# Performance work log

Hardware: AMD Instinct MI355X
Metric: run time of the kernel (lower is better)

Reference implementation:

```python
import jax, jax.numpy as jnp
import numpy as np

VOCAB, EMBED, HIDDEN = 32000, 256, 512
B, T = 8, 512


def setup_inputs() -> dict:
    key = jax.random.key(0)
    ks = jax.random.split(key, 7)
    x = jax.random.randint(ks[0], (B, T), 0, VOCAB)
    emb = jax.random.normal(ks[1], (VOCAB, EMBED), dtype=jnp.float32)
    W_xh = jax.random.normal(ks[2], (EMBED, HIDDEN), dtype=jnp.float32) * 0.01
    W_hh = jax.random.normal(ks[3], (HIDDEN, HIDDEN), dtype=jnp.float32) * 0.01
    b_h = jnp.zeros((HIDDEN,), dtype=jnp.float32)
    # nn.Linear(hidden*2, vocab): weight [vocab, 2*hidden], bias [vocab]
    lim = 1.0 / np.sqrt(2 * HIDDEN)
    fc_w = jax.random.uniform(ks[4], (VOCAB, 2 * HIDDEN), minval=-lim, maxval=lim, dtype=jnp.float32)
    fc_b = jax.random.uniform(ks[5], (VOCAB,), minval=-lim, maxval=lim, dtype=jnp.float32)
    return {"x": x, "emb": emb, "W_xh": W_xh, "W_hh": W_hh, "b_h": b_h, "fc_w": fc_w, "fc_b": fc_b}


def reference(x, emb, W_xh, W_hh, b_h, fc_w, fc_b):
    e = emb[x]  # [B,T,E]
    h0 = jnp.zeros((x.shape[0], W_hh.shape[0]), dtype=e.dtype)

    def step(h, xt):  # xt: [B,E]
        h = jnp.tanh(xt @ W_xh + h @ W_hh + b_h)
        return h, h

    _, H = jax.lax.scan(step, h0, jnp.swapaxes(e, 0, 1))  # H: [T,B,Hd]
    H = jnp.swapaxes(H, 0, 1)  # [B,T,Hd]
    # full (non-causal) dot-product self-attention over hidden states
    scores = jnp.einsum('bth,bsh->bts', H, H)  # [B,T,T]
    attn = jax.nn.softmax(scores, axis=-1)
    ctx = jnp.einsum('bts,bsh->bth', attn, H)  # [B,T,Hd]
    combined = jnp.concatenate([H, ctx], axis=-1)  # [B,T,2Hd]
    return combined @ fc_w.T + fc_b  # [B,T,V]
```

## Files before the change

kernel.cpp:

```cpp
#include <hip/hip_runtime.h>

typedef unsigned int u32;
typedef unsigned short u16;
typedef short bf16x8 __attribute__((ext_vector_type(8)));
typedef float f32x4 __attribute__((ext_vector_type(4)));

#define DEV __device__ __forceinline__

DEV u16 f2bf(float f) {
  u32 u = __builtin_bit_cast(u32, f);
  u += 0x7fffu + ((u >> 16) & 1u);
  return (u16)(u >> 16);
}
DEV float bf2f(u16 b) { u32 u = ((u32)b) << 16; return __builtin_bit_cast(float, u); }

DEV float dot2bf(float acc, u32 w, u32 h) {
  asm("v_dot2_f32_bf16 %0, %1, %2, %0" : "+v"(acc) : "v"(w), "v"(h));
  return acc;
}

DEV void gload16(const void* g, void* l) {
  __builtin_amdgcn_global_load_lds(
      (__attribute__((address_space(1))) void*)(void*)g,
      (__attribute__((address_space(3))) void*)l, 16, 0, 0);
}

__global__ void k_prep_fcw(const float* __restrict__ w, u16* __restrict__ o, int n4) {
  int i = blockIdx.x * blockDim.x + threadIdx.x;
  int stride = gridDim.x * blockDim.x;
  for (; i < n4; i += stride) {
    float4 v = ((const float4*)w)[i];
    ushort4 r; r.x = f2bf(v.x); r.y = f2bf(v.y); r.z = f2bf(v.z); r.w = f2bf(v.w);
    ((ushort4*)o)[i] = r;
  }
}

__global__ void k_prep_whh(const float* __restrict__ w, u32* __restrict__ o) {
  int idx = blockIdx.x * 256 + threadIdx.x;
  int p = idx >> 9, j = idx & 511;
  float lo = w[p * 1024 + j];
  float hi = w[p * 1024 + 512 + j];
  o[idx] = (u32)f2bf(lo) | ((u32)f2bf(hi) << 16);
}

__global__ __launch_bounds__(256) void k_embx(
    const int* __restrict__ x, const float* __restrict__ emb,
    const float* __restrict__ wxh, const float* __restrict__ bh,
    float* __restrict__ X) {
  __shared__ float sA[64][65];
  __shared__ __align__(16) float sB[64][68];
  int tid = threadIdx.x;
  int row0 = blockIdx.x * 64, col0 = blockIdx.y * 64;
  int tx = tid & 15, ty = tid >> 4;
  f32x4 acc[4] = {};
  for (int kc = 0; kc < 256; kc += 64) {
    __syncthreads();
#pragma unroll
    for (int i = 0; i < 4; ++i) {
      int f = i * 256 + tid;
      int r = f >> 4, c4 = (f & 15) * 4;
      int xr = x[row0 + r];
      float4 v = *(const float4*)&emb[(size_t)xr * 256 + kc + c4];
      sA[r][c4 + 0] = v.x; sA[r][c4 + 1] = v.y; sA[r][c4 + 2] = v.z; sA[r][c4 + 3] = v.w;
      float4 u = *(const float4*)&wxh[(size_t)(kc + r) * 512 + col0 + c4];
      *(float4*)&sB[r][c4] = u;
    }
    __syncthreads();
#pragma unroll
    for (int e = 0; e < 64; ++e) {
      f32x4 bv = *(const f32x4*)&sB[e][tx * 4];
      float a0 = sA[ty * 4 + 0][e], a1 = sA[ty * 4 + 1][e];
      float a2 = sA[ty * 4 + 2][e], a3 = sA[ty * 4 + 3][e];
      acc[0] += a0 * bv; acc[1] += a1 * bv; acc[2] += a2 * bv; acc[3] += a3 * bv;
    }
  }
  f32x4 bh4 = *(const f32x4*)&bh[col0 + tx * 4];
#pragma unroll
  for (int a = 0; a < 4; ++a) {
    f32x4 r = acc[a] + bh4;
    *(f32x4*)&X[(size_t)(row0 + ty * 4 + a) * 512 + col0 + tx * 4] = r;
  }
}

#define PREG 216
#define PL   40

__global__ __launch_bounds__(512, 1) void k_rnn(
    const u32* __restrict__ Wpk, const float* __restrict__ X,
    u16* __restrict__ Hb16 ) {
  __shared__ u32 wl[PL * 512];
  __shared__ __align__(16) u32 hHI[2][256];
  __shared__ __align__(16) u32 hLO[2][256];
  int j = threadIdx.x;
  int b = blockIdx.x;
  u32 wreg[PREG];
#pragma unroll
  for (int p = 0; p < PREG; ++p) wreg[p] = Wpk[p * 512 + j];
#pragma unroll
  for (int p = 0; p < PL; ++p) wl[p * 512 + j] = Wpk[(PREG + p) * 512 + j];
  if (j < 256) { hHI[0][j] = 0u; hLO[0][j] = 0u; }
  const float* Xb = X + (size_t)b * 512 * 512;
  u16* Hb = Hb16 + (size_t)b * 512 * 1024;
  __syncthreads();
  int cur = 0;
  for (int t = 0; t < 512; ++t) {
    float xv = Xb[t * 512 + j];
    float a0 = 0.f, a1 = 0.f, a2 = 0.f, a3 = 0.f;
    const u32* hbH = hHI[cur];
    const u32* hbL = hLO[cur];
#pragma unroll
    for (int c = 0; c < PREG / 4; ++c) {
      uint4 hH = *(const uint4*)&hbH[c * 4];
      uint4 hL = *(const uint4*)&hbL[c * 4];
      a0 = dot2bf(dot2bf(a0, wreg[c * 4 + 0], hH.x), wreg[c * 4 + 0], hL.x);
      a1 = dot2bf(dot2bf(a1, wreg[c * 4 + 1], hH.y), wreg[c * 4 + 1], hL.y);
      a2 = dot2bf(dot2bf(a2, wreg[c * 4 + 2], hH.z), wreg[c * 4 + 2], hL.z);
      a3 = dot2bf(dot2bf(a3, wreg[c * 4 + 3], hH.w), wreg[c * 4 + 3], hL.w);
    }
#pragma unroll
    for (int c = 0; c < PL / 4; ++c) {
      uint4 hH = *(const uint4*)&hbH[PREG + c * 4];
      uint4 hL = *(const uint4*)&hbL[PREG + c * 4];
      u32 w0 = wl[(c * 4 + 0) * 512 + j];
      u32 w1 = wl[(c * 4 + 1) * 512 + j];
      u32 w2 = wl[(c * 4 + 2) * 512 + j];
      u32 w3 = wl[(c * 4 + 3) * 512 + j];
      a0 = dot2bf(dot2bf(a0, w0, hH.x), w0, hL.x);
      a1 = dot2bf(dot2bf(a1, w1, hH.y), w1, hL.y);
      a2 = dot2bf(dot2bf(a2, w2, hH.z), w2, hL.z);
      a3 = dot2bf(dot2bf(a3, w3, hH.w), w3, hL.w);
    }
    float z = xv + ((a0 + a1) + (a2 + a3));
    float ez = __expf(2.f * z);
    float h = 1.f - 2.f / (ez + 1.f);
    u16 hi = f2bf(h);
    u16 lo = f2bf(h - bf2f(hi));
    Hb[t * 1024 + j] = hi;
    ((u16*)hHI[cur ^ 1])[j] = hi;
    ((u16*)hLO[cur ^ 1])[j] = lo;
    __syncthreads();
    cur ^= 1;
  }
}

template <int BF16OUT, int BIAS, int BF32B>
__global__ __launch_bounds__(256) void k_gemm_bt(
    const u16* __restrict__ A, int lda, long long aStr,
    const void* __restrict__ Bt_, int ldb, long long bStr,
    void* __restrict__ Cv, int ldc, long long cStr,
    int numMt, int numNt, int K, const float* __restrict__ bias) {
  __shared__ __align__(16) u16 lA[128 * 64];
  __shared__ __align__(16) u16 lB[128 * 64];
  int tid = threadIdx.x;
  int lane = tid & 63, wid = tid >> 6;
  int nwg = gridDim.x, wg = blockIdx.x;
  int q = nwg >> 3;
  int swz = (wg & 7) * q + (wg >> 3);
  int gm = numMt < 8 ? numMt : 8;
  int perg = gm * numNt;
  int grp = swz / perg;
  int rem = swz - grp * perg;
  int mt = grp * gm + rem % gm;
  int nt = rem / gm;
  int mrow = mt * 128, ncol = nt * 128;
  long long batch = blockIdx.y;
  A += batch * aStr;
  const u16* Bh = (const u16*)Bt_ + (BF32B ? 0 : batch * bStr);
  const float* Bf = (const float*)Bt_ + (BF32B ? batch * bStr : 0);
  float* Cf = (float*)Cv + batch * cStr;
  u16* Ch = (u16*)Cv + batch * cStr;

  f32x4 acc[4][4] = {};
  int wr = wid >> 1, wc = wid & 1;
  int lr = lane & 15, lk = (lane >> 4) * 8;

  for (int kt = 0; kt < K; kt += 64) {
    __syncthreads();
#pragma unroll
    for (int i = 0; i < 4; ++i) {
      int chunk = wid * 4 + i;
      int idx = chunk * 64 + lane;
      int r = idx >> 3, c = (idx & 7) * 8;
      gload16(&A[(size_t)(mrow + r) * lda + kt + c], &lA[chunk * 512]);
    }
    if constexpr (!BF32B) {
#pragma unroll
      for (int i = 0; i < 4; ++i) {
        int chunk = wid * 4 + i;
        int idx = chunk * 64 + lane;
        int r = idx >> 3, c = (idx & 7) * 8;
        gload16(&Bh[(size_t)(ncol + r) * ldb + kt + c], &lB[chunk * 512]);
      }
    } else {
#pragma unroll
      for (int u = 0; u < 8; ++u) {
        int flat = u * 1024 + tid * 4;
        int r = flat >> 6, c = flat & 63;
        float4 v = *(const float4*)&Bf[(size_t)(ncol + r) * ldb + kt + c];
        uint2 pk;
        pk.x = (u32)f2bf(v.x) | ((u32)f2bf(v.y) << 16);
        pk.y = (u32)f2bf(v.z) | ((u32)f2bf(v.w) << 16);
        *(uint2*)&lB[r * 64 + c] = pk;
      }
    }
    __syncthreads();
#pragma unroll
    for (int ks = 0; ks < 2; ++ks) {
      bf16x8 aF[4], bF[4];
#pragma unroll
      for (int mi = 0; mi < 4; ++mi)
        aF[mi] = *(const bf16x8*)&lA[(wr * 64 + mi * 16 + lr) * 64 + ks * 32 + lk];
#pragma unroll
      for (int ni = 0; ni < 4; ++ni)
        bF[ni] = *(const bf16x8*)&lB[(wc * 64 + ni * 16 + lr) * 64 + ks * 32 + lk];
#pragma unroll
      for (int mi = 0; mi < 4; ++mi)
#pragma unroll
        for (int ni = 0; ni < 4; ++ni)
          acc[mi][ni] = __builtin_amdgcn_mfma_f32_16x16x32_bf16(aF[mi], bF[ni], acc[mi][ni], 0, 0, 0);
    }
  }
  int rq = (lane >> 4) * 4;
#pragma unroll
  for (int ni = 0; ni < 4; ++ni) {
    int col = ncol + wc * 64 + ni * 16 + lr;
    float bv = BIAS ? bias[col] : 0.f;
#pragma unroll
    for (int mi = 0; mi < 4; ++mi) {
      int row = mrow + wr * 64 + mi * 16 + rq;
#pragma unroll
      for (int qq = 0; qq < 4; ++qq) {
        float v = acc[mi][ni][qq] + bv;
        if (BF16OUT) Ch[(size_t)(row + qq) * ldc + col] = f2bf(v);
        else         Cf[(size_t)(row + qq) * ldc + col] = v;
      }
    }
  }
}

__global__ __launch_bounds__(256) void k_softmax(const float* __restrict__ S, u16* __restrict__ P) {
  int wid = threadIdx.x >> 6, lane = threadIdx.x & 63;
  int row = blockIdx.x * 4 + wid;
  const float* sr = S + (size_t)row * 512;
  f32x4 v0 = *(const f32x4*)&sr[lane * 4];
  f32x4 v1 = *(const f32x4*)&sr[256 + lane * 4];
  float m = fmaxf(fmaxf(fmaxf(v0.x, v0.y), fmaxf(v0.z, v0.w)),
                  fmaxf(fmaxf(v1.x, v1.y), fmaxf(v1.z, v1.w)));
#pragma unroll
  for (int o = 32; o; o >>= 1) m = fmaxf(m, __shfl_xor(m, o, 64));
  f32x4 e0, e1;
  e0.x = __expf(v0.x - m); e0.y = __expf(v0.y - m); e0.z = __expf(v0.z - m); e0.w = __expf(v0.w - m);
  e1.x = __expf(v1.x - m); e1.y = __expf(v1.y - m); e1.z = __expf(v1.z - m); e1.w = __expf(v1.w - m);
  float s = (e0.x + e0.y + e0.z + e0.w) + (e1.x + e1.y + e1.z + e1.w);
#pragma unroll
  for (int o = 32; o; o >>= 1) s += __shfl_xor(s, o, 64);
  float inv = 1.f / s;
  ushort4 o0, o1;
  o0.x = f2bf(e0.x * inv); o0.y = f2bf(e0.y * inv); o0.z = f2bf(e0.z * inv); o0.w = f2bf(e0.w * inv);
  o1.x = f2bf(e1.x * inv); o1.y = f2bf(e1.y * inv); o1.z = f2bf(e1.z * inv); o1.w = f2bf(e1.w * inv);
  *(ushort4*)&P[(size_t)row * 512 + lane * 4] = o0;
  *(ushort4*)&P[(size_t)row * 512 + 256 + lane * 4] = o1;
}

__global__ __launch_bounds__(256) void k_transpose(const u16* __restrict__ Hsrc, u16* __restrict__ HT) {
  __shared__ __align__(16) u16 tile[64][72];
  int b = blockIdx.z;
  int sb = blockIdx.x * 64, hb = blockIdx.y * 64;
  int tid = threadIdx.x;
#pragma unroll
  for (int i = 0; i < 4; ++i) {
    int f = i * 256 + tid; int r = f >> 4, c4 = (f & 15) * 4;
    ushort4 v = *(const ushort4*)&Hsrc[((size_t)(b * 512 + sb + r)) * 1024 + hb + c4];
    *(ushort4*)&tile[r][c4] = v;
  }
  __syncthreads();
#pragma unroll
  for (int i = 0; i < 4; ++i) {
    int f = i * 256 + tid; int h = f >> 4, s4 = (f & 15) * 4;
    ushort4 v;
    v.x = tile[s4 + 0][h]; v.y = tile[s4 + 1][h]; v.z = tile[s4 + 2][h]; v.w = tile[s4 + 3][h];
    *(ushort4*)&HT[((size_t)(b * 512 + hb + h)) * 512 + sb + s4] = v;
  }
}

extern "C" void kernel_launch(void* const* d_in, const int* in_sizes, int n_in,
                              void* d_out, int out_size, void* d_ws, size_t ws_size,
                              hipStream_t stream) {
  const int*   x   = (const int*)d_in[0];
  const float* emb = (const float*)d_in[1];
  const float* wxh = (const float*)d_in[2];
  const float* whh = (const float*)d_in[3];
  const float* bh  = (const float*)d_in[4];
  const float* fcw = (const float*)d_in[5];
  const float* fcb = (const float*)d_in[6];
  float* out = (float*)d_out;

  char* ws = (char*)d_ws;
  u32* whpk = (u32*)ws;
  u16* comb = (u16*)(ws + 524288);
  u16* fcwb = (u16*)(ws + 524288 + 8388608);
  bool bigws = ws_size >= (size_t)(524288 + 8388608 + 65536000);
  char* ob = (char*)d_out;
  float* X  = (float*)ob;
  float* S  = (float*)(ob + 8388608);
  u16*   P  = (u16*)(ob + 16777216);
  u16*   HT = (u16*)(ob + 20971520);

  k_prep_whh<<<dim3(512), dim3(256), 0, stream>>>(whh, whpk);
  k_embx<<<dim3(64, 8), dim3(256), 0, stream>>>(x, emb, wxh, bh, X);
  if (bigws)
    k_prep_fcw<<<dim3(2048), dim3(256), 0, stream>>>(fcw, fcwb, 8192000);
  k_rnn<<<dim3(8), dim3(512), 0, stream>>>(whpk, X, comb);
  k_gemm_bt<0, 0, 0><<<dim3(16, 8), dim3(256), 0, stream>>>(
      comb, 1024, 512LL * 1024, comb, 1024, 512LL * 1024,
      (void*)S, 512, 512LL * 512, 4, 4, 512, (const float*)nullptr);
  k_softmax<<<dim3(1024), dim3(256), 0, stream>>>(S, P);
  k_transpose<<<dim3(8, 8, 8), dim3(256), 0, stream>>>(comb, HT);
  k_gemm_bt<1, 0, 0><<<dim3(16, 8), dim3(256), 0, stream>>>(
      P, 512, 512LL * 512, HT, 512, 512LL * 512,
      (void*)(comb + 512), 1024, 512LL * 1024, 4, 4, 512, (const float*)nullptr);
  if (bigws)
    k_gemm_bt<0, 1, 0><<<dim3(8000), dim3(256), 0, stream>>>(
        comb, 1024, 0LL, fcwb, 1024, 0LL,
        (void*)out, 32000, 0LL, 32, 250, 1024, fcb);
  else
    k_gemm_bt<0, 1, 1><<<dim3(8000), dim3(256), 0, stream>>>(
        comb, 1024, 0LL, fcw, 1024, 0LL,
        (void*)out, 32000, 0LL, 32, 250, 1024, fcb);
}
```

Before: 2.034 ms.

## Repack RNN recurrent weights into vectorized LDS quads and prefetch next input

The recurrent weight split now keeps fewer packed columns in registers (184 instead of 216) and moves the rest into LDS. The LDS part is stored in an interleaved quad layout, so each thread reads four weights with one 128-bit load instead of four scalar loads. The next timestep's X value is loaded before the current step's dot products so its global latency overlaps the compute. This is meant to cut LDS instruction count and register pressure in the serial recurrence, at the cost of more LDS traffic per step and a new occupancy attribute.

```diff
diff --git a/kernel.cpp b/kernel.cpp
--- a/kernel.cpp
+++ b/kernel.cpp
@@ -35,12 +35,15 @@
   }
 }
 
-__global__ void k_prep_whh(const float* __restrict__ w, u32* __restrict__ o) {
+#define PREG 184
+#define PLQ  18
+
+__global__ void k_prep_whh(const float* __restrict__ w, u32* __restrict__ wr, u32* __restrict__ wq) {
   int idx = blockIdx.x * 256 + threadIdx.x;
   int p = idx >> 9, j = idx & 511;
-  float lo = w[p * 1024 + j];
-  float hi = w[p * 1024 + 512 + j];
-  o[idx] = (u32)f2bf(lo) | ((u32)f2bf(hi) << 16);
+  u32 word = (u32)f2bf(w[(2 * p) * 512 + j]) | ((u32)f2bf(w[(2 * p + 1) * 512 + j]) << 16);
+  if (p < PREG) wr[p * 512 + j] = word;
+  else { int d = p - PREG; wq[((d >> 2) * 512 + j) * 4 + (d & 3)] = word; }
 }
 
 __global__ __launch_bounds__(256) void k_embx(
@@ -82,29 +85,32 @@
   }
 }
 
-#define PREG 216
-#define PL   40
-
-__global__ __launch_bounds__(512, 1) void k_rnn(
-    const u32* __restrict__ Wpk, const float* __restrict__ X,
+__global__ __launch_bounds__(512)
+__attribute__((amdgpu_waves_per_eu(2, 2)))
+void k_rnn(
+    const u32* __restrict__ Wr, const u32* __restrict__ Wq,
+    const float* __restrict__ X,
     u16* __restrict__ Hb16 ) {
-  __shared__ u32 wl[PL * 512];
+  __shared__ __align__(16) u32 wl[PLQ * 512 * 4];
   __shared__ __align__(16) u32 hHI[2][256];
   __shared__ __align__(16) u32 hLO[2][256];
   int j = threadIdx.x;
   int b = blockIdx.x;
   u32 wreg[PREG];
 #pragma unroll
-  for (int p = 0; p < PREG; ++p) wreg[p] = Wpk[p * 512 + j];
-#pragma unroll
-  for (int p = 0; p < PL; ++p) wl[p * 512 + j] = Wpk[(PREG + p) * 512 + j];
+  for (int p = 0; p < PREG; ++p) wreg[p] = Wr[p * 512 + j];
+#pragma unroll
+  for (int q = 0; q < PLQ; ++q)
+    *(uint4*)&wl[(q * 512 + j) * 4] = *(const uint4*)&Wq[(q * 512 + j) * 4];
   if (j < 256) { hHI[0][j] = 0u; hLO[0][j] = 0u; }
   const float* Xb = X + (size_t)b * 512 * 512;
   u16* Hb = Hb16 + (size_t)b * 512 * 1024;
   __syncthreads();
   int cur = 0;
+  float xv = Xb[j];
   for (int t = 0; t < 512; ++t) {
-    float xv = Xb[t * 512 + j];
+    int tn = t < 511 ? t + 1 : 511;
+    float xnext = Xb[tn * 512 + j];
     float a0 = 0.f, a1 = 0.f, a2 = 0.f, a3 = 0.f;
     const u32* hbH = hHI[cur];
     const u32* hbL = hLO[cur];
@@ -118,17 +124,14 @@
       a3 = dot2bf(dot2bf(a3, wreg[c * 4 + 3], hH.w), wreg[c * 4 + 3], hL.w);
     }
 #pragma unroll
-    for (int c = 0; c < PL / 4; ++c) {
-      uint4 hH = *(const uint4*)&hbH[PREG + c * 4];
-      uint4 hL = *(const uint4*)&hbL[PREG + c * 4];
-      u32 w0 = wl[(c * 4 + 0) * 512 + j];
-      u32 w1 = wl[(c * 4 + 1) * 512 + j];
-      u32 w2 = wl[(c * 4 + 2) * 512 + j];
-      u32 w3 = wl[(c * 4 + 3) * 512 + j];
-      a0 = dot2bf(dot2bf(a0, w0, hH.x), w0, hL.x);
-      a1 = dot2bf(dot2bf(a1, w1, hH.y), w1, hL.y);
-      a2 = dot2bf(dot2bf(a2, w2, hH.z), w2, hL.z);
-      a3 = dot2bf(dot2bf(a3, w3, hH.w), w3, hL.w);
+    for (int q = 0; q < PLQ; ++q) {
+      uint4 wv = *(const uint4*)&wl[(q * 512 + j) * 4];
+      uint4 hH = *(const uint4*)&hbH[PREG + q * 4];
+      uint4 hL = *(const uint4*)&hbL[PREG + q * 4];
+      a0 = dot2bf(dot2bf(a0, wv.x, hH.x), wv.x, hL.x);
+      a1 = dot2bf(dot2bf(a1, wv.y, hH.y), wv.y, hL.y);
+      a2 = dot2bf(dot2bf(a2, wv.z, hH.z), wv.z, hL.z);
+      a3 = dot2bf(dot2bf(a3, wv.w, hH.w), wv.w, hL.w);
     }
     float z = xv + ((a0 + a1) + (a2 + a3));
     float ez = __expf(2.f * z);
@@ -140,6 +143,7 @@
     ((u16*)hLO[cur ^ 1])[j] = lo;
     __syncthreads();
     cur ^= 1;
+    xv = xnext;
   }
 }
 
@@ -296,7 +300,8 @@
   float* out = (float*)d_out;
 
   char* ws = (char*)d_ws;
-  u32* whpk = (u32*)ws;
+  u32* Wr  = (u32*)ws;
+  u32* Wq  = (u32*)(ws + 376832);
   u16* comb = (u16*)(ws + 524288);
   u16* fcwb = (u16*)(ws + 524288 + 8388608);
   bool bigws = ws_size >= (size_t)(524288 + 8388608 + 65536000);
@@ -306,11 +311,11 @@
   u16*   P  = (u16*)(ob + 16777216);
   u16*   HT = (u16*)(ob + 20971520);
 
-  k_prep_whh<<<dim3(512), dim3(256), 0, stream>>>(whh, whpk);
+  k_prep_whh<<<dim3(512), dim3(256), 0, stream>>>(whh, Wr, Wq);
   k_embx<<<dim3(64, 8), dim3(256), 0, stream>>>(x, emb, wxh, bh, X);
   if (bigws)
     k_prep_fcw<<<dim3(2048), dim3(256), 0, stream>>>(fcw, fcwb, 8192000);
-  k_rnn<<<dim3(8), dim3(512), 0, stream>>>(whpk, X, comb);
+  k_rnn<<<dim3(8), dim3(512), 0, stream>>>(Wr, Wq, X, comb);
   k_gemm_bt<0, 0, 0><<<dim3(16, 8), dim3(256), 0, stream>>>(
       comb, 1024, 512LL * 1024, comb, 1024, 512LL * 1024,
       (void*)S, 512, 512LL * 512, 4, 4, 512, (const float*)nullptr);
```

Result: faster. 1.797 ms (-11.7%).

## Rewrite RNN recurrence with MFMA over all batches in one block

Applied to the files above, without the earlier changes.

Replaces the per-batch dot2-based recurrent matvec with a single-block MFMA formulation. The 8 batches' hi and lo bf16 parts of h form the 16 rows of the A operand, and the two halves are combined via a cross-lane shuffle. W_hh is pre-packed into MFMA fragment layout, mostly kept in registers, with one column tile streamed from memory each step. The next step's X is prefetched into LDS asynchronously. The aim is to cut per-step serial latency of the recurrence, at the cost of using a single CU and reloading part of the weights every step.

```diff
diff --git a/kernel.cpp b/kernel.cpp
--- a/kernel.cpp
+++ b/kernel.cpp
@@ -13,11 +13,6 @@
   return (u16)(u >> 16);
 }
 DEV float bf2f(u16 b) { u32 u = ((u32)b) << 16; return __builtin_bit_cast(float, u); }
-
-DEV float dot2bf(float acc, u32 w, u32 h) {
-  asm("v_dot2_f32_bf16 %0, %1, %2, %0" : "+v"(acc) : "v"(w), "v"(h));
-  return acc;
-}
 
 DEV void gload16(const void* g, void* l) {
   __builtin_amdgcn_global_load_lds(
@@ -35,12 +30,20 @@
   }
 }
 
-__global__ void k_prep_whh(const float* __restrict__ w, u32* __restrict__ o) {
-  int idx = blockIdx.x * 256 + threadIdx.x;
-  int p = idx >> 9, j = idx & 511;
-  float lo = w[p * 1024 + j];
-  float hi = w[p * 1024 + 512 + j];
-  o[idx] = (u32)f2bf(lo) | ((u32)f2bf(hi) << 16);
+__global__ void k_prep_wfrag(const float* __restrict__ w, u16* __restrict__ o) {
+  int t = blockIdx.x * 256 + threadIdx.x;
+  int c = t >> 10, s = (t >> 6) & 15, l = t & 63;
+  int kb = s * 32 + ((l >> 4) * 8);
+  int col = c * 16 + (l & 15);
+  u16 v[8];
+#pragma unroll
+  for (int j = 0; j < 8; ++j) v[j] = f2bf(w[(size_t)(kb + j) * 512 + col]);
+  uint4 pk;
+  pk.x = (u32)v[0] | ((u32)v[1] << 16);
+  pk.y = (u32)v[2] | ((u32)v[3] << 16);
+  pk.z = (u32)v[4] | ((u32)v[5] << 16);
+  pk.w = (u32)v[6] | ((u32)v[7] << 16);
+  ((uint4*)o)[t] = pk;
 }
 
 __global__ __launch_bounds__(256) void k_embx(
@@ -82,62 +85,104 @@
   }
 }
 
-#define PREG 216
-#define PL   40
-
-__global__ __launch_bounds__(512, 1) void k_rnn(
-    const u32* __restrict__ Wpk, const float* __restrict__ X,
-    u16* __restrict__ Hb16 ) {
-  __shared__ u32 wl[PL * 512];
-  __shared__ __align__(16) u32 hHI[2][256];
-  __shared__ __align__(16) u32 hLO[2][256];
-  int j = threadIdx.x;
-  int b = blockIdx.x;
-  u32 wreg[PREG];
-#pragma unroll
-  for (int p = 0; p < PREG; ++p) wreg[p] = Wpk[p * 512 + j];
-#pragma unroll
-  for (int p = 0; p < PL; ++p) wl[p * 512 + j] = Wpk[(PREG + p) * 512 + j];
-  if (j < 256) { hHI[0][j] = 0u; hLO[0][j] = 0u; }
-  const float* Xb = X + (size_t)b * 512 * 512;
-  u16* Hb = Hb16 + (size_t)b * 512 * 1024;
+__global__ __launch_bounds__(512, 2) void k_rnn_mfma(
+    const u16* __restrict__ Wpk, const float* __restrict__ X,
+    u16* __restrict__ comb ) {
+  __shared__ u16 h2[2][16][520];
+  __shared__ __align__(16) float xs[2][4096];
+  int tid = threadIdx.x, lane = tid & 63, w = tid >> 6;
+
+  bf16x8 bf[3][16];
+#pragma unroll
+  for (int ci = 0; ci < 3; ++ci)
+#pragma unroll
+    for (int s = 0; s < 16; ++s)
+      bf[ci][s] = *(const bf16x8*)&Wpk[((size_t)(((4 * w + ci) * 16 + s) * 64) + lane) * 8];
+
+  for (int i = tid; i < 4160; i += 512) ((u32*)&h2[0][0][0])[i] = 0u;
+
+  {
+    int f0 = ((w * 2 + 0) * 64 + lane) * 4;
+    gload16(&X[(size_t)(f0 >> 9) * 262144 + (f0 & 511)], &xs[0][(w * 2 + 0) * 256]);
+    int f1 = ((w * 2 + 1) * 64 + lane) * 4;
+    gload16(&X[(size_t)(f1 >> 9) * 262144 + (f1 & 511)], &xs[0][(w * 2 + 1) * 256]);
+  }
   __syncthreads();
+
+  const u16* wsb = Wpk + (size_t)((4 * w + 3) * 16) * 512;
+  int ard = (lane & 15) * 520 + (lane >> 4) * 8;
   int cur = 0;
+
   for (int t = 0; t < 512; ++t) {
-    float xv = Xb[t * 512 + j];
-    float a0 = 0.f, a1 = 0.f, a2 = 0.f, a3 = 0.f;
-    const u32* hbH = hHI[cur];
-    const u32* hbL = hLO[cur];
-#pragma unroll
-    for (int c = 0; c < PREG / 4; ++c) {
-      uint4 hH = *(const uint4*)&hbH[c * 4];
-      uint4 hL = *(const uint4*)&hbL[c * 4];
-      a0 = dot2bf(dot2bf(a0, wreg[c * 4 + 0], hH.x), wreg[c * 4 + 0], hL.x);
-      a1 = dot2bf(dot2bf(a1, wreg[c * 4 + 1], hH.y), wreg[c * 4 + 1], hL.y);
-      a2 = dot2bf(dot2bf(a2, wreg[c * 4 + 2], hH.z), wreg[c * 4 + 2], hL.z);
-      a3 = dot2bf(dot2bf(a3, wreg[c * 4 + 3], hH.w), wreg[c * 4 + 3], hL.w);
-    }
-#pragma unroll
-    for (int c = 0; c < PL / 4; ++c) {
-      uint4 hH = *(const uint4*)&hbH[PREG + c * 4];
-      uint4 hL = *(const uint4*)&hbL[PREG + c * 4];
-      u32 w0 = wl[(c * 4 + 0) * 512 + j];
-      u32 w1 = wl[(c * 4 + 1) * 512 + j];
-      u32 w2 = wl[(c * 4 + 2) * 512 + j];
-      u32 w3 = wl[(c * 4 + 3) * 512 + j];
-      a0 = dot2bf(dot2bf(a0, w0, hH.x), w0, hL.x);
-      a1 = dot2bf(dot2bf(a1, w1, hH.y), w1, hL.y);
-      a2 = dot2bf(dot2bf(a2, w2, hH.z), w2, hL.z);
-      a3 = dot2bf(dot2bf(a3, w3, hH.w), w3, hL.w);
-    }
-    float z = xv + ((a0 + a1) + (a2 + a3));
-    float ez = __expf(2.f * z);
-    float h = 1.f - 2.f / (ez + 1.f);
-    u16 hi = f2bf(h);
-    u16 lo = f2bf(h - bf2f(hi));
-    Hb[t * 1024 + j] = hi;
-    ((u16*)hHI[cur ^ 1])[j] = hi;
-    ((u16*)hLO[cur ^ 1])[j] = lo;
+    int tn = t < 511 ? t + 1 : 511;
+    {
+      int f0 = ((w * 2 + 0) * 64 + lane) * 4;
+      gload16(&X[(size_t)(f0 >> 9) * 262144 + (size_t)tn * 512 + (f0 & 511)],
+              &xs[cur ^ 1][(w * 2 + 0) * 256]);
+      int f1 = ((w * 2 + 1) * 64 + lane) * 4;
+      gload16(&X[(size_t)(f1 >> 9) * 262144 + (size_t)tn * 512 + (f1 & 511)],
+              &xs[cur ^ 1][(w * 2 + 1) * 256]);
+    }
+    f32x4 acc[4];
+    if (lane < 32) {
+#pragma unroll
+      for (int ci = 0; ci < 4; ++ci) {
+        int colg = (4 * w + ci) * 16 + (lane & 15);
+#pragma unroll
+        for (int r = 0; r < 4; ++r)
+          acc[ci][r] = xs[cur][((lane >> 4) * 4 + r) * 512 + colg];
+      }
+    } else {
+#pragma unroll
+      for (int ci = 0; ci < 4; ++ci)
+#pragma unroll
+        for (int r = 0; r < 4; ++r) acc[ci][r] = 0.f;
+    }
+    bf16x8 bs[16];
+#pragma unroll
+    for (int s = 0; s < 8; ++s) bs[s] = *(const bf16x8*)&wsb[s * 512 + lane * 8];
+    const u16* hrd = &h2[cur][0][0];
+#pragma unroll
+    for (int s = 0; s < 16; ++s) {
+      if (s == 4) {
+#pragma unroll
+        for (int q = 8; q < 12; ++q) bs[q] = *(const bf16x8*)&wsb[q * 512 + lane * 8];
+      }
+      if (s == 8) {
+#pragma unroll
+        for (int q = 12; q < 16; ++q) bs[q] = *(const bf16x8*)&wsb[q * 512 + lane * 8];
+      }
+      bf16x8 af = *(const bf16x8*)&hrd[ard + s * 32];
+      acc[0] = __builtin_amdgcn_mfma_f32_16x16x32_bf16(af, bf[0][s], acc[0], 0, 0, 0);
+      acc[1] = __builtin_amdgcn_mfma_f32_16x16x32_bf16(af, bf[1][s], acc[1], 0, 0, 0);
+      acc[2] = __builtin_amdgcn_mfma_f32_16x16x32_bf16(af, bf[2][s], acc[2], 0, 0, 0);
+      acc[3] = __builtin_amdgcn_mfma_f32_16x16x32_bf16(af, bs[s], acc[3], 0, 0, 0);
+    }
+    float z[4][4];
+#pragma unroll
+    for (int ci = 0; ci < 4; ++ci)
+#pragma unroll
+      for (int r = 0; r < 4; ++r)
+        z[ci][r] = acc[ci][r] + __shfl_xor(acc[ci][r], 32, 64);
+    if (lane < 32) {
+      u16* hwn = &h2[cur ^ 1][0][0];
+#pragma unroll
+      for (int ci = 0; ci < 4; ++ci) {
+        int colg = (4 * w + ci) * 16 + (lane & 15);
+#pragma unroll
+        for (int r = 0; r < 4; ++r) {
+          int b = (lane >> 4) * 4 + r;
+          float zz = z[ci][r];
+          float e = __expf(2.f * zz);
+          float h = 1.f - 2.f / (e + 1.f);
+          u16 hi = f2bf(h);
+          u16 lo = f2bf(h - bf2f(hi));
+          hwn[b * 520 + colg] = hi;
+          hwn[(8 + b) * 520 + colg] = lo;
+          comb[((size_t)(b * 512 + t)) * 1024 + colg] = hi;
+        }
+      }
+    }
     __syncthreads();
     cur ^= 1;
   }
@@ -296,7 +341,7 @@
   float* out = (float*)d_out;
 
   char* ws = (char*)d_ws;
-  u32* whpk = (u32*)ws;
+  u16* Wpk = (u16*)ws;
   u16* comb = (u16*)(ws + 524288);
   u16* fcwb = (u16*)(ws + 524288 + 8388608);
   bool bigws = ws_size >= (size_t)(524288 + 8388608 + 65536000);
@@ -306,11 +351,11 @@
   u16*   P  = (u16*)(ob + 16777216);
   u16*   HT = (u16*)(ob + 20971520);
 
-  k_prep_whh<<<dim3(512), dim3(256), 0, stream>>>(whh, whpk);
+  k_prep_wfrag<<<dim3(128), dim3(256), 0, stream>>>(whh, Wpk);
   k_embx<<<dim3(64, 8), dim3(256), 0, stream>>>(x, emb, wxh, bh, X);
   if (bigws)
     k_prep_fcw<<<dim3(2048), dim3(256), 0, stream>>>(fcw, fcwb, 8192000);
-  k_rnn<<<dim3(8), dim3(512), 0, stream>>>(whpk, X, comb);
+  k_rnn_mfma<<<dim3(1), dim3(512), 0, stream>>>(Wpk, X, comb);
   k_gemm_bt<0, 0, 0><<<dim3(16, 8), dim3(256), 0, stream>>>(
       comb, 1024, 512LL * 1024, comb, 1024, 512LL * 1024,
       (void*)S, 512, 512LL * 512, 4, 4, 512, (const float*)nullptr);
```

After: 3.387 ms. 1.66x slower.
